# Optimization experiments

Measured on AMD Instinct MI355X. Metric: run time of the kernel, lower is better.

Reference implementation:

```python
import jax, jax.numpy as jnp
import numpy as np

N_NODES = 20000
N_EDGES = 40000
H = 64          # n_hidden
F_ATOM = 62     # n_atom_features (< H, triggers zero-pad path)
F_BOND = 6      # n_bond_features
B = 512         # number of graphs in batch
T = 2           # message passing steps


def setup_inputs() -> dict:
    key = jax.random.key(0)
    ks = jax.random.split(key, 20)
    s = 0.05  # small init scale to avoid selu/tanh saturation
    inp = {
        'node_features': jax.random.normal(ks[0], (N_NODES, F_ATOM), jnp.float32),
        'edge_features': jax.random.normal(ks[1], (N_EDGES, F_BOND), jnp.float32),
        'edge_domain': jax.random.randint(ks[2], (N_EDGES,), 0, N_NODES, jnp.int32),
        'edge_range': jax.random.randint(ks[3], (N_EDGES,), 0, N_NODES, jnp.int32),
        'graph_id': jnp.sort(jax.random.randint(ks[4], (N_NODES,), 0, B, jnp.int32)),
        # EdgeNetwork params (weights stored [in, out], i.e. torch W.T)
        'Wm': jax.random.normal(ks[5], (F_BOND, H), jnp.float32) * s,
        'bm': jnp.zeros((H,), jnp.float32),
        'Ew': jax.random.normal(ks[6], (H, H * H), jnp.float32) * s,  # E.weight used as mm(mlp, E.weight): [H, H*H]
        # update2 linears (T=2)
        'Wu0': jax.random.normal(ks[7], (H, H), jnp.float32) * s,
        'bu0': jnp.zeros((H,), jnp.float32),
        'Wu1': jax.random.normal(ks[8], (H, H), jnp.float32) * s,
        'bu1': jnp.zeros((H,), jnp.float32),
        # atom_embed
        'Wae': jax.random.normal(ks[9], (H, H), jnp.float32) * s,
        'bae': jnp.zeros((H,), jnp.float32),
        # AggregateReadout.R
        'WR': jax.random.normal(ks[10], (H, H), jnp.float32) * s,
        'bR': jnp.zeros((H,), jnp.float32),
        # mlp + out head
        'Wmlp': jax.random.normal(ks[11], (H, H), jnp.float32) * s,
        'bmlp': jnp.zeros((H,), jnp.float32),
        'Wout': jax.random.normal(ks[12], (H, 1), jnp.float32) * s,
        'bout': jnp.zeros((1,), jnp.float32),
    }
    return inp


def reference(node_features, edge_features, edge_domain, edge_range, graph_id,
              Wm, bm, Ew, Wu0, bu0, Wu1, bu1, Wae, bae, WR, bR,
              Wmlp, bmlp, Wout, bout):
    # pad node features up to n_hidden (original zero-pads when narrower)
    h = jnp.pad(node_features, ((0, 0), (0, H - F_ATOM)))  # [N, H]

    # EdgeNetwork: edge-conditioned per-edge HxH weight matrix.
    # Edge features are constant across T, so A is identical each step;
    # compute once (original recomputes the same values every iteration).
    mlp_features = jax.nn.relu(edge_features @ Wm + bm)      # [E, H]
    A = (mlp_features @ Ew).reshape(-1, H, H)                # [E, H, H]

    for Wu, bu in ((Wu0, bu0), (Wu1, bu1)):
        hj = h[edge_range]                                   # gather [E, H]
        edge_message = jnp.einsum('eij,ej->ei', A, hj)       # bmm [E, H]
        message = jax.ops.segment_sum(edge_message, edge_domain,
                                      num_segments=N_NODES)  # scatter-add [N, H]
        h = jax.nn.selu(message @ Wu + bu + h)

    atom_embedding = h @ Wae + bae                           # [N, H]
    # AggregateReadout
    atom_activation = jax.nn.selu(atom_embedding @ WR + bR)  # [N, H]
    graph_sum = jax.ops.segment_sum(atom_activation, graph_id, num_segments=B)
    graph_embedding = jnp.tanh(graph_sum)                    # [B, H]

    mlp_out = jax.nn.relu(graph_embedding @ Wmlp + bmlp)     # [B, H]
    out = mlp_out @ Wout + bout                              # [B, 1]
    return out.reshape(-1, 1)
```

## Files before the change

### kernel.cpp

```cpp
#include <hip/hip_runtime.h>
#include <math.h>

#define NN 20000
#define NE 40000
#define H 64
#define F_ATOM 62
#define F_BOND 6
#define NB 512

typedef _Float16 f16x8 __attribute__((ext_vector_type(8)));
typedef float f32x16 __attribute__((ext_vector_type(16)));

__device__ __forceinline__ float selu_f(float x) {
    const float scale = 1.0507009873554805f;
    const float alpha = 1.6732632423543772f;
    return scale * (x > 0.0f ? x : alpha * (__expf(x) - 1.0f));
}

__device__ __forceinline__ f16x8 splat8h(_Float16 x) {
    union { _Float16 h[2]; unsigned u; } p;
    p.h[0] = x; p.h[1] = x;
    union { unsigned u[4]; f16x8 v; } r;
    r.u[0] = p.u; r.u[1] = p.u; r.u[2] = p.u; r.u[3] = p.u;
    return r.v;
}

__global__ void prep_kernel(const float* __restrict__ nf, const float* __restrict__ ef,
                            const float* __restrict__ Wm, const float* __restrict__ bm,
                            const float* __restrict__ Ew,
                            _Float16* __restrict__ h_h,
                            unsigned* __restrict__ mlp2, _Float16* __restrict__ ewb,
                            float* __restrict__ msg, float* __restrict__ gsum) {
    const int bid = blockIdx.x;
    const int t = threadIdx.x;
    if (bid < 625) {
        __shared__ float st[64][65];
        const int el = t & 63;
        const int ig = t >> 6;
        const int e = bid * 64 + el;
        const float* efe = ef + e * F_BOND;
        const float e0 = efe[0], e1 = efe[1], e2 = efe[2];
        const float e3 = efe[3], e4 = efe[4], e5 = efe[5];
#pragma unroll
        for (int p = 0; p < 16; ++p) {
            const int i = ig * 16 + p;
            float s = bm[i];
            s = fmaf(e0, Wm[0 * H + i], s);
            s = fmaf(e1, Wm[1 * H + i], s);
            s = fmaf(e2, Wm[2 * H + i], s);
            s = fmaf(e3, Wm[3 * H + i], s);
            s = fmaf(e4, Wm[4 * H + i], s);
            s = fmaf(e5, Wm[5 * H + i], s);
            st[i][el] = fmaxf(s, 0.0f);
        }
        __syncthreads();
        const int p = t >> 3;
        const int ch = t & 7;
#pragma unroll
        for (int j = 0; j < 8; ++j) {
            const int e_l = ch * 8 + j;
            union { unsigned u; _Float16 hh[2]; } pk;
            pk.hh[0] = (_Float16)st[2 * p][e_l];
            pk.hh[1] = (_Float16)st[2 * p + 1][e_l];
            mlp2[(size_t)p * NE + bid * 64 + e_l] = pk.u;
        }
    } else if (bid < 5625) {
        int idx = (bid - 625) * 256 + t;
        int n = idx >> 6, c = idx & 63;
        h_h[idx] = (_Float16)((c < F_ATOM) ? nf[n * F_ATOM + c] : 0.0f);
    } else if (bid < 5753) {
        int tid = (bid - 5625) * 256 + t;
        int l = tid & 63;
        int nt = (tid >> 6) & 1;
        int c = tid >> 7;
        int kk = c >> 2;
        int jbase = (c & 3) * 16 + (l >> 5) * 8;
        int i = nt * 32 + (l & 31);
        const float* src = Ew + kk * 4096 + i * 64 + jbase;
        _Float16* dst = ewb + tid * 8;
#pragma unroll
        for (int u = 0; u < 8; ++u) dst[u] = (_Float16)src[u];
    } else if (bid < 7003) {
        int idx = (bid - 5753) * 256 + t;
        reinterpret_cast<float4*>(msg)[idx] = make_float4(0.f, 0.f, 0.f, 0.f);
    } else {
        int idx = (bid - 7003) * 256 + t;
        reinterpret_cast<float4*>(gsum)[idx] = make_float4(0.f, 0.f, 0.f, 0.f);
    }
}

__global__ __launch_bounds__(128, 2) void edge_message_mfma(
    const _Float16* __restrict__ h_h, const unsigned* __restrict__ mlp2,
    const int* __restrict__ ed, const int* __restrict__ er,
    const _Float16* __restrict__ ewb, float* __restrict__ msg)
{
    __shared__ char sm[49152];
    __shared__ int edom_s[64];

    const int t = threadIdx.x;
    const int lane = t & 63;
    const int kg = t >> 6;
    const int l31 = lane & 31;
    const int hf = lane >> 5;
    const int eb = blockIdx.x * 64;

    if (t < 64) edom_s[t] = ed[eb + t];

    const int eA = eb + l31;
    const int eB = eA + 32;
    const int gA = er[eA], gB = er[eB];

    f16x8 hjA[4], hjB[4];
#pragma unroll
    for (int cq = 0; cq < 4; ++cq) {
        hjA[cq] = *reinterpret_cast<const f16x8*>(h_h + gA * 64 + cq * 16 + hf * 8);
        hjB[cq] = *reinterpret_cast<const f16x8*>(h_h + gB * 64 + cq * 16 + hf * 8);
    }

    unsigned mvA[16], mvB[16];
#pragma unroll
    for (int pp = 0; pp < 16; ++pp) {
        mvA[pp] = mlp2[(size_t)(kg * 16 + pp) * NE + eA];
        mvB[pp] = mlp2[(size_t)(kg * 16 + pp) * NE + eB];
    }

    asm volatile("s_waitcnt vmcnt(0)" ::: "memory");

    char* wbase = sm + kg * 24576;
    auto stage = [&](int s) {
        const char* gs = reinterpret_cast<const char*>(ewb) +
                         ((size_t)(kg * 32 + s) << 13) + lane * 16;
        char* lb = wbase + (s % 3) * 8192 + lane * 16;
#pragma unroll
        for (int r = 0; r < 8; ++r) {
            __builtin_amdgcn_global_load_lds(
                (const __attribute__((address_space(1))) void*)(gs + r * 1024),
                (__attribute__((address_space(3))) void*)(lb + r * 1024),
                16, 0, 0);
        }
    };

    f32x16 a00, a01, a10, a11;
#pragma unroll
    for (int i = 0; i < 16; ++i) { a00[i] = 0.f; a01[i] = 0.f; a10[i] = 0.f; a11[i] = 0.f; }

    stage(0);
    stage(1);

#pragma unroll
    for (int s = 0; s < 32; ++s) {
        if (s < 31) asm volatile("s_waitcnt vmcnt(8)" ::: "memory");
        else        asm volatile("s_waitcnt vmcnt(0)" ::: "memory");
        if (s < 30) stage(s + 2);
        const char* buf = wbase + (s % 3) * 8192;
        union { unsigned u; _Float16 hh[2]; } ua, ub;
        ua.u = mvA[s >> 1]; ub.u = mvB[s >> 1];
        f16x8 sA = splat8h(ua.hh[s & 1]);
        f16x8 sB = splat8h(ub.hh[s & 1]);
        __builtin_amdgcn_s_setprio(1);
#pragma unroll
        for (int cq = 0; cq < 4; ++cq) {
            f16x8 b0 = *reinterpret_cast<const f16x8*>(buf + (cq * 2 + 0) * 1024 + lane * 16);
            f16x8 b1 = *reinterpret_cast<const f16x8*>(buf + (cq * 2 + 1) * 1024 + lane * 16);
            f16x8 aA = sA * hjA[cq];
            f16x8 aB = sB * hjB[cq];
            a00 = __builtin_amdgcn_mfma_f32_32x32x16_f16(aA, b0, a00, 0, 0, 0);
            a01 = __builtin_amdgcn_mfma_f32_32x32x16_f16(aA, b1, a01, 0, 0, 0);
            a10 = __builtin_amdgcn_mfma_f32_32x32x16_f16(aB, b0, a10, 0, 0, 0);
            a11 = __builtin_amdgcn_mfma_f32_32x32x16_f16(aB, b1, a11, 0, 0, 0);
        }
        __builtin_amdgcn_s_setprio(0);
    }

    float* X = reinterpret_cast<float*>(sm);
    __syncthreads();
    if (kg == 1) {
#pragma unroll
        for (int r = 0; r < 16; ++r) {
            const int m = (r & 3) + 8 * (r >> 2) + 4 * hf;
            X[m * 64 + l31]             = a00[r];
            X[m * 64 + 32 + l31]        = a01[r];
            X[(32 + m) * 64 + l31]      = a10[r];
            X[(32 + m) * 64 + 32 + l31] = a11[r];
        }
    }
    __syncthreads();
    if (kg == 0) {
#pragma unroll
        for (int r = 0; r < 16; ++r) {
            const int m = (r & 3) + 8 * (r >> 2) + 4 * hf;
            const int domA = edom_s[m];
            const int domB = edom_s[32 + m];
            atomicAdd(&msg[domA * 64 + l31],      a00[r] + X[m * 64 + l31]);
            atomicAdd(&msg[domA * 64 + 32 + l31], a01[r] + X[m * 64 + 32 + l31]);
            atomicAdd(&msg[domB * 64 + l31],      a10[r] + X[(32 + m) * 64 + l31]);
            atomicAdd(&msg[domB * 64 + 32 + l31], a11[r] + X[(32 + m) * 64 + 32 + l31]);
        }
    }
}

__global__ __launch_bounds__(256) void node_update_kernel(
    float* __restrict__ msg, const float* __restrict__ Wu,
    const float* __restrict__ bu, _Float16* __restrict__ h_h) {
    __shared__ float ms[32][65];
    const int t = threadIdx.x;
    const int nb = blockIdx.x * 32;
#pragma unroll
    for (int r = 0; r < 2; ++r) {
        int idx = r * 256 + t;
        int n = idx >> 4, c4 = (idx & 15) * 4;
        float4* src = reinterpret_cast<float4*>(msg + (size_t)(nb + n) * 64 + c4);
        float4 v = *src;
        *src = make_float4(0.f, 0.f, 0.f, 0.f);
        ms[n][c4 + 0] = v.x; ms[n][c4 + 1] = v.y;
        ms[n][c4 + 2] = v.z; ms[n][c4 + 3] = v.w;
    }
    __syncthreads();
    const int i = t & 63;
    const int n0 = (t >> 6) * 8;
    float acc[8];
#pragma unroll
    for (int j = 0; j < 8; ++j) acc[j] = bu[i];
#pragma unroll 8
    for (int k = 0; k < 64; ++k) {
        float w = Wu[k * 64 + i];
#pragma unroll
        for (int j = 0; j < 8; ++j) acc[j] = fmaf(ms[n0 + j][k], w, acc[j]);
    }
#pragma unroll
    for (int j = 0; j < 8; ++j) {
        int o = (nb + n0 + j) * 64 + i;
        h_h[o] = (_Float16)selu_f(acc[j] + (float)h_h[o]);
    }
}

__global__ __launch_bounds__(256) void upd2_embed_readout(
    const float* __restrict__ msg, const float* __restrict__ Wu,
    const float* __restrict__ bu, const _Float16* __restrict__ h_h,
    const float* __restrict__ Wae, const float* __restrict__ bae,
    const float* __restrict__ WR, const float* __restrict__ bR,
    const int* __restrict__ gid, float* __restrict__ gsum) {
    __shared__ float ms[32][65];
    __shared__ float hn[32][65];
    __shared__ float ae[32][65];
    const int t = threadIdx.x;
    const int nb = blockIdx.x * 32;
#pragma unroll
    for (int r = 0; r < 2; ++r) {
        int idx = r * 256 + t;
        int n = idx >> 4, c4 = (idx & 15) * 4;
        float4 v = *reinterpret_cast<const float4*>(msg + (size_t)(nb + n) * 64 + c4);
        ms[n][c4 + 0] = v.x; ms[n][c4 + 1] = v.y;
        ms[n][c4 + 2] = v.z; ms[n][c4 + 3] = v.w;
    }
    __syncthreads();
    const int i = t & 63;
    const int n0 = (t >> 6) * 8;
    float acc[8];
#pragma unroll
    for (int j = 0; j < 8; ++j) acc[j] = bu[i];
#pragma unroll 8
    for (int k = 0; k < 64; ++k) {
        float w = Wu[k * 64 + i];
#pragma unroll
        for (int j = 0; j < 8; ++j) acc[j] = fmaf(ms[n0 + j][k], w, acc[j]);
    }
#pragma unroll
    for (int j = 0; j < 8; ++j)
        hn[n0 + j][i] = selu_f(acc[j] + (float)h_h[(nb + n0 + j) * 64 + i]);
    __syncthreads();
#pragma unroll
    for (int j = 0; j < 8; ++j) acc[j] = bae[i];
#pragma unroll 8
    for (int k = 0; k < 64; ++k) {
        float w = Wae[k * 64 + i];
#pragma unroll
        for (int j = 0; j < 8; ++j) acc[j] = fmaf(hn[n0 + j][k], w, acc[j]);
    }
#pragma unroll
    for (int j = 0; j < 8; ++j) ae[n0 + j][i] = acc[j];
    __syncthreads();
#pragma unroll
    for (int j = 0; j < 8; ++j) acc[j] = bR[i];
#pragma unroll 8
    for (int k = 0; k < 64; ++k) {
        float w = WR[k * 64 + i];
#pragma unroll
        for (int j = 0; j < 8; ++j) acc[j] = fmaf(ae[n0 + j][k], w, acc[j]);
    }
#pragma unroll
    for (int j = 0; j < 8; ++j)
        atomicAdd(&gsum[gid[nb + n0 + j] * 64 + i], selu_f(acc[j]));
}

__global__ void final_kernel(const float* __restrict__ gsum, const float* __restrict__ Wmlp,
                             const float* __restrict__ bmlp, const float* __restrict__ Wout,
                             const float* __restrict__ bout, float* __restrict__ out) {
    __shared__ float ge[64];
    int g = blockIdx.x, i = threadIdx.x;
    ge[i] = tanhf(gsum[g * H + i]);
    __syncthreads();
    float s = bmlp[i];
#pragma unroll
    for (int k = 0; k < H; ++k) s = fmaf(ge[k], Wmlp[k * H + i], s);
    float mo = fmaxf(s, 0.0f) * Wout[i];
#pragma unroll
    for (int off = 32; off > 0; off >>= 1) mo += __shfl_down(mo, off);
    if (i == 0) out[g] = mo + bout[0];
}

extern "C" void kernel_launch(void* const* d_in, const int* in_sizes, int n_in,
                              void* d_out, int out_size, void* d_ws, size_t ws_size,
                              hipStream_t stream) {
    const float* nf   = (const float*)d_in[0];
    const float* ef   = (const float*)d_in[1];
    const int*   ed   = (const int*)d_in[2];
    const int*   er   = (const int*)d_in[3];
    const int*   gid  = (const int*)d_in[4];
    const float* Wm   = (const float*)d_in[5];
    const float* bm   = (const float*)d_in[6];
    const float* Ew   = (const float*)d_in[7];
    const float* Wu0  = (const float*)d_in[8];
    const float* bu0  = (const float*)d_in[9];
    const float* Wu1  = (const float*)d_in[10];
    const float* bu1  = (const float*)d_in[11];
    const float* Wae  = (const float*)d_in[12];
    const float* bae  = (const float*)d_in[13];
    const float* WR   = (const float*)d_in[14];
    const float* bR   = (const float*)d_in[15];
    const float* Wmlp = (const float*)d_in[16];
    const float* bmlp = (const float*)d_in[17];
    const float* Wout = (const float*)d_in[18];
    const float* bout = (const float*)d_in[19];
    float* out = (float*)d_out;

    float* ws = (float*)d_ws;
    float*    msg  = ws + 1280000;
    float*    gsum = ws + 2560000;
    unsigned* mlp2 = (unsigned*)(ws + 2592768);
    _Float16* h_h  = (_Float16*)(ws + 3872768);
    _Float16* ewb  = (_Float16*)(ws + 4512768);

    prep_kernel<<<7035, 256, 0, stream>>>(nf, ef, Wm, bm, Ew, h_h, mlp2, ewb, msg, gsum);

    edge_message_mfma<<<625, 128, 0, stream>>>(h_h, mlp2, ed, er, ewb, msg);
    node_update_kernel<<<NN / 32, 256, 0, stream>>>(msg, Wu0, bu0, h_h);
    edge_message_mfma<<<625, 128, 0, stream>>>(h_h, mlp2, ed, er, ewb, msg);
    upd2_embed_readout<<<NN / 32, 256, 0, stream>>>(msg, Wu1, bu1, h_h,
                                                    Wae, bae, WR, bR, gid, gsum);

    final_kernel<<<NB, 64, 0, stream>>>(gsum, Wmlp, bmlp, Wout, bout, out);
}
```

Measured before the change: 113.8 us.

## Tile edge-message kernel over 128 edges with split-K across block pairs

Result: slower. 139.9 us (+22.9%).

```diff
diff --git a/kernel.cpp b/kernel.cpp
--- a/kernel.cpp
+++ b/kernel.cpp
@@ -95,33 +95,46 @@
     const _Float16* __restrict__ ewb, float* __restrict__ msg)
 {
     __shared__ char sm[49152];
-    __shared__ int edom_s[64];
+    __shared__ int edom_s[128];
 
     const int t = threadIdx.x;
     const int lane = t & 63;
     const int kg = t >> 6;
     const int l31 = lane & 31;
     const int hf = lane >> 5;
-    const int eb = blockIdx.x * 64;
-
-    if (t < 64) edom_s[t] = ed[eb + t];
+    const int kh = blockIdx.x & 1;
+    const int eb = (blockIdx.x >> 1) * 128;
+    const int kbase = kh * 32 + kg * 16;
+
+    if (t < 128) { int ee = eb + t; edom_s[t] = ed[ee < NE ? ee : NE - 1]; }
 
     const int eA = eb + l31;
     const int eB = eA + 32;
-    const int gA = er[eA], gB = er[eB];
-
-    f16x8 hjA[4], hjB[4];
+    const int eC = eA + 64;
+    const int eD = eA + 96;
+    const int eAc = eA < NE ? eA : NE - 1;
+    const int eBc = eB < NE ? eB : NE - 1;
+    const int eCc = eC < NE ? eC : NE - 1;
+    const int eDc = eD < NE ? eD : NE - 1;
+    const int gA = er[eAc], gB = er[eBc], gC = er[eCc], gD = er[eDc];
+
+    f16x8 hjA[4], hjB[4], hjC[4], hjD[4];
 #pragma unroll
     for (int cq = 0; cq < 4; ++cq) {
         hjA[cq] = *reinterpret_cast<const f16x8*>(h_h + gA * 64 + cq * 16 + hf * 8);
         hjB[cq] = *reinterpret_cast<const f16x8*>(h_h + gB * 64 + cq * 16 + hf * 8);
-    }
-
-    unsigned mvA[16], mvB[16];
-#pragma unroll
-    for (int pp = 0; pp < 16; ++pp) {
-        mvA[pp] = mlp2[(size_t)(kg * 16 + pp) * NE + eA];
-        mvB[pp] = mlp2[(size_t)(kg * 16 + pp) * NE + eB];
+        hjC[cq] = *reinterpret_cast<const f16x8*>(h_h + gC * 64 + cq * 16 + hf * 8);
+        hjD[cq] = *reinterpret_cast<const f16x8*>(h_h + gD * 64 + cq * 16 + hf * 8);
+    }
+
+    unsigned mvA[8], mvB[8], mvC[8], mvD[8];
+#pragma unroll
+    for (int pp = 0; pp < 8; ++pp) {
+        const size_t o = (size_t)((kbase >> 1) + pp) * NE;
+        mvA[pp] = mlp2[o + eAc];
+        mvB[pp] = mlp2[o + eBc];
+        mvC[pp] = mlp2[o + eCc];
+        mvD[pp] = mlp2[o + eDc];
     }
 
     asm volatile("s_waitcnt vmcnt(0)" ::: "memory");
@@ -129,7 +142,7 @@
     char* wbase = sm + kg * 24576;
     auto stage = [&](int s) {
         const char* gs = reinterpret_cast<const char*>(ewb) +
-                         ((size_t)(kg * 32 + s) << 13) + lane * 16;
+                         ((size_t)(kbase + s) << 13) + lane * 16;
         char* lb = wbase + (s % 3) * 8192 + lane * 16;
 #pragma unroll
         for (int r = 0; r < 8; ++r) {
@@ -140,34 +153,46 @@
         }
     };
 
-    f32x16 a00, a01, a10, a11;
-#pragma unroll
-    for (int i = 0; i < 16; ++i) { a00[i] = 0.f; a01[i] = 0.f; a10[i] = 0.f; a11[i] = 0.f; }
+    f32x16 a00, a01, a10, a11, a20, a21, a30, a31;
+#pragma unroll
+    for (int i = 0; i < 16; ++i) {
+        a00[i] = 0.f; a01[i] = 0.f; a10[i] = 0.f; a11[i] = 0.f;
+        a20[i] = 0.f; a21[i] = 0.f; a30[i] = 0.f; a31[i] = 0.f;
+    }
 
     stage(0);
     stage(1);
 
 #pragma unroll
-    for (int s = 0; s < 32; ++s) {
-        if (s < 31) asm volatile("s_waitcnt vmcnt(8)" ::: "memory");
+    for (int s = 0; s < 16; ++s) {
+        if (s < 15) asm volatile("s_waitcnt vmcnt(8)" ::: "memory");
         else        asm volatile("s_waitcnt vmcnt(0)" ::: "memory");
-        if (s < 30) stage(s + 2);
+        if (s < 14) stage(s + 2);
         const char* buf = wbase + (s % 3) * 8192;
-        union { unsigned u; _Float16 hh[2]; } ua, ub;
-        ua.u = mvA[s >> 1]; ub.u = mvB[s >> 1];
-        f16x8 sA = splat8h(ua.hh[s & 1]);
-        f16x8 sB = splat8h(ub.hh[s & 1]);
+        union { unsigned u; _Float16 hh[2]; } u0, u1, u2, u3;
+        u0.u = mvA[s >> 1]; u1.u = mvB[s >> 1];
+        u2.u = mvC[s >> 1]; u3.u = mvD[s >> 1];
+        f16x8 s0 = splat8h(u0.hh[s & 1]);
+        f16x8 s1 = splat8h(u1.hh[s & 1]);
+        f16x8 s2 = splat8h(u2.hh[s & 1]);
+        f16x8 s3 = splat8h(u3.hh[s & 1]);
         __builtin_amdgcn_s_setprio(1);
 #pragma unroll
         for (int cq = 0; cq < 4; ++cq) {
             f16x8 b0 = *reinterpret_cast<const f16x8*>(buf + (cq * 2 + 0) * 1024 + lane * 16);
             f16x8 b1 = *reinterpret_cast<const f16x8*>(buf + (cq * 2 + 1) * 1024 + lane * 16);
-            f16x8 aA = sA * hjA[cq];
-            f16x8 aB = sB * hjB[cq];
+            f16x8 aA = s0 * hjA[cq];
+            f16x8 aB = s1 * hjB[cq];
+            f16x8 aC = s2 * hjC[cq];
+            f16x8 aD = s3 * hjD[cq];
             a00 = __builtin_amdgcn_mfma_f32_32x32x16_f16(aA, b0, a00, 0, 0, 0);
             a01 = __builtin_amdgcn_mfma_f32_32x32x16_f16(aA, b1, a01, 0, 0, 0);
             a10 = __builtin_amdgcn_mfma_f32_32x32x16_f16(aB, b0, a10, 0, 0, 0);
             a11 = __builtin_amdgcn_mfma_f32_32x32x16_f16(aB, b1, a11, 0, 0, 0);
+            a20 = __builtin_amdgcn_mfma_f32_32x32x16_f16(aC, b0, a20, 0, 0, 0);
+            a21 = __builtin_amdgcn_mfma_f32_32x32x16_f16(aC, b1, a21, 0, 0, 0);
+            a30 = __builtin_amdgcn_mfma_f32_32x32x16_f16(aD, b0, a30, 0, 0, 0);
+            a31 = __builtin_amdgcn_mfma_f32_32x32x16_f16(aD, b1, a31, 0, 0, 0);
         }
         __builtin_amdgcn_s_setprio(0);
     }
@@ -178,10 +203,14 @@
 #pragma unroll
         for (int r = 0; r < 16; ++r) {
             const int m = (r & 3) + 8 * (r >> 2) + 4 * hf;
-            X[m * 64 + l31]             = a00[r];
-            X[m * 64 + 32 + l31]        = a01[r];
-            X[(32 + m) * 64 + l31]      = a10[r];
-            X[(32 + m) * 64 + 32 + l31] = a11[r];
+            X[m * 64 + l31]              = a00[r];
+            X[m * 64 + 32 + l31]         = a01[r];
+            X[(32 + m) * 64 + l31]       = a10[r];
+            X[(32 + m) * 64 + 32 + l31]  = a11[r];
+            X[(64 + m) * 64 + l31]       = a20[r];
+            X[(64 + m) * 64 + 32 + l31]  = a21[r];
+            X[(96 + m) * 64 + l31]       = a30[r];
+            X[(96 + m) * 64 + 32 + l31]  = a31[r];
         }
     }
     __syncthreads();
@@ -189,12 +218,27 @@
 #pragma unroll
         for (int r = 0; r < 16; ++r) {
             const int m = (r & 3) + 8 * (r >> 2) + 4 * hf;
-            const int domA = edom_s[m];
-            const int domB = edom_s[32 + m];
-            atomicAdd(&msg[domA * 64 + l31],      a00[r] + X[m * 64 + l31]);
-            atomicAdd(&msg[domA * 64 + 32 + l31], a01[r] + X[m * 64 + 32 + l31]);
-            atomicAdd(&msg[domB * 64 + l31],      a10[r] + X[(32 + m) * 64 + l31]);
-            atomicAdd(&msg[domB * 64 + 32 + l31], a11[r] + X[(32 + m) * 64 + 32 + l31]);
+            const int mA = m, mB = 32 + m, mC = 64 + m, mD = 96 + m;
+            if (eb + mA < NE) {
+                const int dom = edom_s[mA];
+                atomicAdd(&msg[dom * 64 + l31],      a00[r] + X[mA * 64 + l31]);
+                atomicAdd(&msg[dom * 64 + 32 + l31], a01[r] + X[mA * 64 + 32 + l31]);
+            }
+            if (eb + mB < NE) {
+                const int dom = edom_s[mB];
+                atomicAdd(&msg[dom * 64 + l31],      a10[r] + X[mB * 64 + l31]);
+                atomicAdd(&msg[dom * 64 + 32 + l31], a11[r] + X[mB * 64 + 32 + l31]);
+            }
+            if (eb + mC < NE) {
+                const int dom = edom_s[mC];
+                atomicAdd(&msg[dom * 64 + l31],      a20[r] + X[mC * 64 + l31]);
+                atomicAdd(&msg[dom * 64 + 32 + l31], a21[r] + X[mC * 64 + 32 + l31]);
+            }
+            if (eb + mD < NE) {
+                const int dom = edom_s[mD];
+                atomicAdd(&msg[dom * 64 + l31],      a30[r] + X[mD * 64 + l31]);
+                atomicAdd(&msg[dom * 64 + 32 + l31], a31[r] + X[mD * 64 + 32 + l31]);
+            }
         }
     }
 }
@@ -343,9 +387,9 @@
 
     prep_kernel<<<7035, 256, 0, stream>>>(nf, ef, Wm, bm, Ew, h_h, mlp2, ewb, msg, gsum);
 
-    edge_message_mfma<<<625, 128, 0, stream>>>(h_h, mlp2, ed, er, ewb, msg);
+    edge_message_mfma<<<626, 128, 0, stream>>>(h_h, mlp2, ed, er, ewb, msg);
     node_update_kernel<<<NN / 32, 256, 0, stream>>>(msg, Wu0, bu0, h_h);
-    edge_message_mfma<<<625, 128, 0, stream>>>(h_h, mlp2, ed, er, ewb, msg);
+    edge_message_mfma<<<626, 128, 0, stream>>>(h_h, mlp2, ed, er, ewb, msg);
     upd2_embed_readout<<<NN / 32, 256, 0, stream>>>(msg, Wu1, bu1, h_h,
                                                     Wae, bae, WR, bR, gid, gsum);
 
```

## Split edge-message K reduction across four waves and vectorize h_h padding

Applied to the files above, without the earlier changes.

Measured after the change: 116.3 us. 2.1% more time.

```diff
diff --git a/kernel.cpp b/kernel.cpp
--- a/kernel.cpp
+++ b/kernel.cpp
@@ -64,12 +64,17 @@
             pk.hh[1] = (_Float16)st[2 * p + 1][e_l];
             mlp2[(size_t)p * NE + bid * 64 + e_l] = pk.u;
         }
-    } else if (bid < 5625) {
-        int idx = (bid - 625) * 256 + t;
-        int n = idx >> 6, c = idx & 63;
-        h_h[idx] = (_Float16)((c < F_ATOM) ? nf[n * F_ATOM + c] : 0.0f);
-    } else if (bid < 5753) {
-        int tid = (bid - 5625) * 256 + t;
+    } else if (bid < 1250) {
+        const int gid8 = ((bid - 625) * 256 + t) * 8;
+        const int n = gid8 >> 6, c0 = gid8 & 63;
+        union { f16x8 v; _Float16 hh[8]; } o;
+        const float* src = nf + (size_t)n * F_ATOM + c0;
+#pragma unroll
+        for (int u = 0; u < 8; ++u)
+            o.hh[u] = (c0 + u < F_ATOM) ? (_Float16)src[u] : (_Float16)0.0f;
+        *reinterpret_cast<f16x8*>(h_h + gid8) = o.v;
+    } else if (bid < 1378) {
+        int tid = (bid - 1250) * 256 + t;
         int l = tid & 63;
         int nt = (tid >> 6) & 1;
         int c = tid >> 7;
@@ -80,16 +85,16 @@
         _Float16* dst = ewb + tid * 8;
 #pragma unroll
         for (int u = 0; u < 8; ++u) dst[u] = (_Float16)src[u];
-    } else if (bid < 7003) {
-        int idx = (bid - 5753) * 256 + t;
+    } else if (bid < 2628) {
+        int idx = (bid - 1378) * 256 + t;
         reinterpret_cast<float4*>(msg)[idx] = make_float4(0.f, 0.f, 0.f, 0.f);
     } else {
-        int idx = (bid - 7003) * 256 + t;
+        int idx = (bid - 2628) * 256 + t;
         reinterpret_cast<float4*>(gsum)[idx] = make_float4(0.f, 0.f, 0.f, 0.f);
     }
 }
 
-__global__ __launch_bounds__(128, 2) void edge_message_mfma(
+__global__ __launch_bounds__(256, 2) void edge_message_mfma(
     const _Float16* __restrict__ h_h, const unsigned* __restrict__ mlp2,
     const int* __restrict__ ed, const int* __restrict__ er,
     const _Float16* __restrict__ ewb, float* __restrict__ msg)
@@ -103,6 +108,7 @@
     const int l31 = lane & 31;
     const int hf = lane >> 5;
     const int eb = blockIdx.x * 64;
+    const int kbase = kg * 16;
 
     if (t < 64) edom_s[t] = ed[eb + t];
 
@@ -117,22 +123,22 @@
         hjB[cq] = *reinterpret_cast<const f16x8*>(h_h + gB * 64 + cq * 16 + hf * 8);
     }
 
-    unsigned mvA[16], mvB[16];
-#pragma unroll
-    for (int pp = 0; pp < 16; ++pp) {
-        mvA[pp] = mlp2[(size_t)(kg * 16 + pp) * NE + eA];
-        mvB[pp] = mlp2[(size_t)(kg * 16 + pp) * NE + eB];
+    unsigned mvA[8], mvB[8];
+#pragma unroll
+    for (int pp = 0; pp < 8; ++pp) {
+        mvA[pp] = mlp2[(size_t)(kg * 8 + pp) * NE + eA];
+        mvB[pp] = mlp2[(size_t)(kg * 8 + pp) * NE + eB];
     }
 
     asm volatile("s_waitcnt vmcnt(0)" ::: "memory");
 
-    char* wbase = sm + kg * 24576;
+    char* wbase = sm + kg * 12288;
     auto stage = [&](int s) {
         const char* gs = reinterpret_cast<const char*>(ewb) +
-                         ((size_t)(kg * 32 + s) << 13) + lane * 16;
-        char* lb = wbase + (s % 3) * 8192 + lane * 16;
-#pragma unroll
-        for (int r = 0; r < 8; ++r) {
+                         ((size_t)(kbase + (s >> 1)) << 13) + ((s & 1) << 12) + lane * 16;
+        char* lb = wbase + (s % 3) * 4096 + lane * 16;
+#pragma unroll
+        for (int r = 0; r < 4; ++r) {
             __builtin_amdgcn_global_load_lds(
                 (const __attribute__((address_space(1))) void*)(gs + r * 1024),
                 (__attribute__((address_space(3))) void*)(lb + r * 1024),
@@ -149,19 +155,20 @@
 
 #pragma unroll
     for (int s = 0; s < 32; ++s) {
-        if (s < 31) asm volatile("s_waitcnt vmcnt(8)" ::: "memory");
+        if (s < 31) asm volatile("s_waitcnt vmcnt(4)" ::: "memory");
         else        asm volatile("s_waitcnt vmcnt(0)" ::: "memory");
         if (s < 30) stage(s + 2);
-        const char* buf = wbase + (s % 3) * 8192;
+        const char* buf = wbase + (s % 3) * 4096;
         union { unsigned u; _Float16 hh[2]; } ua, ub;
-        ua.u = mvA[s >> 1]; ub.u = mvB[s >> 1];
-        f16x8 sA = splat8h(ua.hh[s & 1]);
-        f16x8 sB = splat8h(ub.hh[s & 1]);
+        ua.u = mvA[s >> 2]; ub.u = mvB[s >> 2];
+        f16x8 sA = splat8h(ua.hh[(s >> 1) & 1]);
+        f16x8 sB = splat8h(ub.hh[(s >> 1) & 1]);
         __builtin_amdgcn_s_setprio(1);
 #pragma unroll
-        for (int cq = 0; cq < 4; ++cq) {
-            f16x8 b0 = *reinterpret_cast<const f16x8*>(buf + (cq * 2 + 0) * 1024 + lane * 16);
-            f16x8 b1 = *reinterpret_cast<const f16x8*>(buf + (cq * 2 + 1) * 1024 + lane * 16);
+        for (int cqh = 0; cqh < 2; ++cqh) {
+            const int cq = (s & 1) * 2 + cqh;
+            f16x8 b0 = *reinterpret_cast<const f16x8*>(buf + cqh * 2048 + lane * 16);
+            f16x8 b1 = *reinterpret_cast<const f16x8*>(buf + cqh * 2048 + 1024 + lane * 16);
             f16x8 aA = sA * hjA[cq];
             f16x8 aB = sB * hjB[cq];
             a00 = __builtin_amdgcn_mfma_f32_32x32x16_f16(aA, b0, a00, 0, 0, 0);
@@ -173,6 +180,39 @@
     }
 
     float* X = reinterpret_cast<float*>(sm);
+    float* Y = reinterpret_cast<float*>(sm + 16384);
+    __syncthreads();
+    if (kg >= 2) {
+        float* M = (kg == 2) ? X : Y;
+#pragma unroll
+        for (int r = 0; r < 16; ++r) {
+            const int m = (r & 3) + 8 * (r >> 2) + 4 * hf;
+            M[m * 64 + l31]             = a00[r];
+            M[m * 64 + 32 + l31]        = a01[r];
+            M[(32 + m) * 64 + l31]      = a10[r];
+            M[(32 + m) * 64 + 32 + l31] = a11[r];
+        }
+    }
+    __syncthreads();
+    if (kg == 0) {
+#pragma unroll
+        for (int r = 0; r < 16; ++r) {
+            const int m = (r & 3) + 8 * (r >> 2) + 4 * hf;
+            a00[r] += X[m * 64 + l31];
+            a01[r] += X[m * 64 + 32 + l31];
+            a10[r] += X[(32 + m) * 64 + l31];
+            a11[r] += X[(32 + m) * 64 + 32 + l31];
+        }
+    } else if (kg == 1) {
+#pragma unroll
+        for (int r = 0; r < 16; ++r) {
+            const int m = (r & 3) + 8 * (r >> 2) + 4 * hf;
+            a00[r] += Y[m * 64 + l31];
+            a01[r] += Y[m * 64 + 32 + l31];
+            a10[r] += Y[(32 + m) * 64 + l31];
+            a11[r] += Y[(32 + m) * 64 + 32 + l31];
+        }
+    }
     __syncthreads();
     if (kg == 1) {
 #pragma unroll
@@ -341,11 +381,11 @@
     _Float16* h_h  = (_Float16*)(ws + 3872768);
     _Float16* ewb  = (_Float16*)(ws + 4512768);
 
-    prep_kernel<<<7035, 256, 0, stream>>>(nf, ef, Wm, bm, Ew, h_h, mlp2, ewb, msg, gsum);
-
-    edge_message_mfma<<<625, 128, 0, stream>>>(h_h, mlp2, ed, er, ewb, msg);
+    prep_kernel<<<2660, 256, 0, stream>>>(nf, ef, Wm, bm, Ew, h_h, mlp2, ewb, msg, gsum);
+
+    edge_message_mfma<<<625, 256, 0, stream>>>(h_h, mlp2, ed, er, ewb, msg);
     node_update_kernel<<<NN / 32, 256, 0, stream>>>(msg, Wu0, bu0, h_h);
-    edge_message_mfma<<<625, 128, 0, stream>>>(h_h, mlp2, ed, er, ewb, msg);
+    edge_message_mfma<<<625, 256, 0, stream>>>(h_h, mlp2, ed, er, ewb, msg);
     upd2_embed_readout<<<NN / 32, 256, 0, stream>>>(msg, Wu1, bu1, h_h,
                                                     Wae, bae, WR, bR, gid, gsum);
 
```
